# Performance work log

Hardware: AMD Instinct MI355X
Metric: run time of the kernel (lower is better)

Reference implementation:

```python
import jax, jax.numpy as jnp
import numpy as np

B, S, D, H, KD, HID = 8, 1024, 512, 8, 64, 32


def setup_inputs() -> dict:
    key = jax.random.key(0)
    ks = jax.random.split(key, 13)
    s = 0.05
    return {
        "src": jax.random.normal(ks[0], (B, S, D), jnp.float32),
        "Wq": jax.random.normal(ks[1], (H, KD, D), jnp.float32) * s,
        "Wk": jax.random.normal(ks[2], (H, KD, D), jnp.float32) * s,
        "Wv": jax.random.normal(ks[3], (H, KD, D), jnp.float32) * s,
        "c_raw": jnp.ones((H,), jnp.float32),              # nn.Parameter(1.0) per head
        "L": jnp.full((H,), 2.0, jnp.float32),             # nn.Parameter(2.0) per head
        "w1": jax.random.normal(ks[4], (H, HID), jnp.float32) * s,   # Linear(1,HID) weight
        "b1": jax.random.normal(ks[5], (H, HID), jnp.float32) * s,
        "W2": jax.random.normal(ks[6], (H, HID, HID), jnp.float32) * s,  # [out,in]
        "b2": jax.random.normal(ks[7], (H, HID), jnp.float32) * s,
        "w3": jax.random.normal(ks[8], (H, HID), jnp.float32) * s,   # Linear(HID,1) weight
        "b3": jax.random.normal(ks[9], (H,), jnp.float32) * s,
        "Wo": jax.random.normal(ks[10], (D, D), jnp.float32) * s,
    }


def _gelu(x):
    return jax.nn.gelu(x, approximate=False)  # torch nn.GELU default (erf)


def reference(src, Wq, Wk, Wv, c_raw, L, w1, b1, W2, b2, w3, b3, Wo):
    Bc, Sc, Dc = src.shape
    Hh, Kd = Wq.shape[0], Wq.shape[1]
    # ---- FIRE bias: raw[i,j] = log1p(c*(i-j)) / log1p(c*max(L, i+1)) for j<i else 0
    ii = jnp.arange(Sc, dtype=jnp.float32)[:, None]   # [S,1]
    jj = jnp.arange(Sc, dtype=jnp.float32)[None, :]   # [1,S]
    d = ii - jj                                       # [S,S]
    c = jax.nn.softplus(c_raw)[:, None, None]         # [H,1,1]
    num = jnp.log1p(c * jnp.where(d > 0, d, 1.0)[None])          # safe for d<=0
    den = jnp.log1p(c * jnp.maximum(L[:, None, None], ii[None] + 1.0))
    raw = jnp.where(d[None] > 0, num / den, 0.0)      # [H,S,S]
    # ---- f_theta MLP applied elementwise (Linear(1,h)->GELU->Linear(h,h)->GELU->Linear(h,1))
    h1 = _gelu(raw[..., None] * w1[:, None, None, :] + b1[:, None, None, :])   # [H,S,S,HID]
    h2 = _gelu(jnp.einsum('hijk,hlk->hijl', h1, W2) + b2[:, None, None, :])    # [H,S,S,HID]
    bias = jnp.einsum('hijk,hk->hij', h2, w3) + b3[:, None, None]              # [H,S,S]
    # ---- causal mask (strict upper triangle -> -inf)
    causal = jnp.arange(Sc)[None, :] > jnp.arange(Sc)[:, None]
    bias = jnp.where(causal[None], -jnp.inf, bias)
    # ---- attention per head
    q = jnp.einsum('bsd,hkd->bhsk', src, Wq)
    k = jnp.einsum('bsd,hkd->bhsk', src, Wk)
    v = jnp.einsum('bsd,hkd->bhsk', src, Wv)
    logits = jnp.einsum('bhik,bhjk->bhij', q, k) / jnp.sqrt(jnp.float32(Kd)) + bias[None]
    attn = jax.nn.softmax(logits, axis=-1)
    o = jnp.einsum('bhij,bhjk->bhik', attn, v)        # [B,H,S,KD]
    o = jnp.transpose(o, (0, 2, 1, 3)).reshape(Bc, Sc, Hh * Kd)  # concat heads
    return o @ Wo.T
```

## Files before the change

### kernel.cpp

```cpp
#include <hip/hip_runtime.h>
#include <math.h>

#define S_LEN 1024
#define NHEAD 8
#define BATCH 8
#define KDIM  64
#define HID   32
#define NT    2048
#define LOG2E 1.4426950408889634f
#define TRI(q) ((q) * ((q) + 1) / 2)
#define PERM(m) (((m) & 0x20) | (((m) & 0x0C) << 1) | (((m) & 0x10) >> 2) | ((m) & 3))
#define SWZ(row) (((((row) >> 3) & 1) << 2) | ((row) & 3))

typedef __attribute__((ext_vector_type(8))) short bf16x8;
typedef __attribute__((ext_vector_type(4))) float f32x4;
typedef unsigned short ushort_t;

__device__ inline ushort_t f2bf(float f) {
  union { float f; unsigned u; } v; v.f = f;
  unsigned u = v.u;
  return (ushort_t)((u + 0x7FFFu + ((u >> 16) & 1u)) >> 16);
}
__device__ inline float bf2f(ushort_t u) {
  union { unsigned x; float f; } v; v.x = ((unsigned)u) << 16; return v.f;
}

__device__ inline void gl_lds16(const ushort_t* g, ushort_t* l) {
  __builtin_amdgcn_global_load_lds(
      (const __attribute__((address_space(1))) unsigned int*)g,
      (__attribute__((address_space(3))) unsigned int*)l, 16, 0, 0);
}

__global__ __launch_bounds__(256) void prep(
    const float* __restrict__ s, const float* __restrict__ wq,
    const float* __restrict__ wk, const float* __restrict__ wv,
    const float* __restrict__ wo,
    ushort_t* __restrict__ sb, ushort_t* __restrict__ wqb,
    ushort_t* __restrict__ wkb, ushort_t* __restrict__ wvb,
    ushort_t* __restrict__ wob,
    const float* __restrict__ c_raw, const float* __restrict__ Lp,
    const float* __restrict__ w1, const float* __restrict__ b1,
    const float* __restrict__ W2, const float* __restrict__ b2,
    const float* __restrict__ w3, const float* __restrict__ b3,
    float* __restrict__ num_g, float* __restrict__ rden_g,
    float* __restrict__ gtab_g) {
  __shared__ float h1s[8][33];
  const int bx = blockIdx.x;
  const int tid = threadIdx.x;
  if (bx < 5120) {
    const float* src; ushort_t* dst; int base; float scale = 1.0f;
    if (bx < 4096)      { src = s;  dst = sb;  base = bx; }
    else if (bx < 4352) { src = wq; dst = wqb; base = bx - 4096; scale = 0.125f * LOG2E; }
    else if (bx < 4608) { src = wk; dst = wkb; base = bx - 4352; }
    else if (bx < 4864) { src = wv; dst = wvb; base = bx - 4608; }
    else                { src = wo; dst = wob; base = bx - 4864; }
    const int i = (base * 256 + tid) * 4;
    float4 v = *(const float4*)&src[i];
    ushort4 o;
    o.x = f2bf(v.x * scale); o.y = f2bf(v.y * scale);
    o.z = f2bf(v.z * scale); o.w = f2bf(v.w * scale);
    *(ushort4*)&dst[i] = o;
  } else {
    const int idx = bx - 5120;
    const int h = idx / 257;
    const int xb = idx % 257;
    const float cr = c_raw[h];
    const float c = (cr > 20.f) ? cr : log1pf(expf(cr));
    const int gid = xb * 256 + tid;
    if (gid < S_LEN) {
      num_g[h * S_LEN + gid] = log1pf(c * (float)gid);
      rden_g[h * S_LEN + gid] = 1.0f / log1pf(c * fmaxf(Lp[h], (float)(gid + 1)));
    }
    const int pl = tid >> 5;
    const int j = tid & 31;
    const int pt = xb * 8 + pl;
    const float x = (float)pt * (1.0f / NT);
    float v = x * w1[h * HID + j] + b1[h * HID + j];
    h1s[pl][j] = 0.5f * v * (1.0f + erff(v * 0.70710678118f));
    __syncthreads();
    float sm = b2[h * HID + j];
    const float* w2r = W2 + ((size_t)(h * HID + j)) * HID;
    #pragma unroll
    for (int k = 0; k < HID; ++k) sm += w2r[k] * h1s[pl][k];
    float g = 0.5f * sm * (1.0f + erff(sm * 0.70710678118f));
    float y = w3[h * HID + j] * g;
    #pragma unroll
    for (int off = 1; off < 32; off <<= 1) y += __shfl_xor(y, off);
    if (j == 0 && pt <= NT) gtab_g[h * (NT + 1) + pt] = (y + b3[h]) * LOG2E;
  }
}

__device__ __forceinline__ void gemm_tile(
    ushort_t* sAB, const ushort_t* __restrict__ A, const ushort_t* __restrict__ Wp,
    void* __restrict__ outp, int mode, int m0, int n0, int tid) {
  const int lane = tid & 63, w = tid >> 6, quad = lane >> 4, l16 = lane & 15;
  f32x4 acc[4];
  #pragma unroll
  for (int nb = 0; nb < 4; ++nb) acc[nb] = (f32x4)0.0f;

  const int r8 = lane >> 3;
  const int gc = (lane & 7) ^ r8;
  const int sw = l16 & 7;

  auto stage = [&](int kt, int buf) {
    ushort_t* sA = sAB + buf * 8192;
    ushort_t* sB = sA + 4096;
    #pragma unroll
    for (int j = 0; j < 2; ++j) {
      const int row = w * 16 + j * 8 + r8;
      gl_lds16(&A[(size_t)(m0 + row) * 512 + kt + gc * 8], &sA[(w * 16 + j * 8) * 64]);
      gl_lds16(&Wp[(size_t)(n0 + row) * 512 + kt + gc * 8], &sB[(w * 16 + j * 8) * 64]);
    }
  };

  stage(0, 0);
  __syncthreads();
  for (int kt8 = 0; kt8 < 8; ++kt8) {
    const int cur = kt8 & 1;
    if (kt8 < 7) stage((kt8 + 1) * 64, cur ^ 1);
    const ushort_t* sA = sAB + cur * 8192;
    const ushort_t* sB = sA + 4096;
    #pragma unroll
    for (int ks = 0; ks < 2; ++ks) {
      const int off = ((ks * 4 + quad) ^ sw) * 8;
      bf16x8 af = *(const bf16x8*)&sA[(w * 16 + l16) * 64 + off];
      #pragma unroll
      for (int nb = 0; nb < 4; ++nb) {
        bf16x8 bfr = *(const bf16x8*)&sB[(nb * 16 + l16) * 64 + off];
        acc[nb] = __builtin_amdgcn_mfma_f32_16x16x32_bf16(af, bfr, acc[nb], 0, 0, 0);
      }
    }
    __syncthreads();
  }

  if (mode == 2) {
    #pragma unroll
    for (int nb = 0; nb < 4; ++nb)
      #pragma unroll
      for (int r = 0; r < 4; ++r) {
        int nl = nb * 16 + l16;
        int ml = w * 16 + quad * 4 + r;
        sAB[nl * 64 + (((ml >> 3) ^ (nl & 7)) * 8) + (ml & 7)] = f2bf(acc[nb][r]);
      }
    __syncthreads();
    const int nl = tid >> 2, seg = tid & 3;
    const int ng = n0 + nl, hh = ng >> 6, kd = ng & 63;
    const int bb = m0 >> 10, sbase = m0 & 1023;
    ushort_t* vout = (ushort_t*)outp + (((size_t)(bb * NHEAD + hh)) * KDIM + kd) * S_LEN;
    #pragma unroll
    for (int c2 = 0; c2 < 2; ++c2) {
      int mc = seg * 2 + c2;
      bf16x8 vr = *(bf16x8*)&sAB[nl * 64 + ((mc ^ (nl & 7)) * 8)];
      *(bf16x8*)&vout[sbase + mc * 8] = vr;
    }
    return;
  }
  #pragma unroll
  for (int nb = 0; nb < 4; ++nb) {
    #pragma unroll
    for (int r = 0; r < 4; ++r) {
      int m = m0 + w * 16 + quad * 4 + r;
      int n = n0 + nb * 16 + l16;
      float v = acc[nb][r];
      if (mode == 1) {
        int bb = m >> 10, ss = m & 1023, hh = n >> 6, kd = n & 63;
        ((ushort_t*)outp)[(((size_t)(bb * NHEAD + hh)) * S_LEN + ss) * KDIM + kd] = f2bf(v);
      } else {
        ((float*)outp)[(size_t)m * 512 + n] = v;
      }
    }
  }
}

__global__ __launch_bounds__(256) void gemm_bias(
    const ushort_t* __restrict__ A,
    const ushort_t* __restrict__ W0, const ushort_t* __restrict__ W1,
    const ushort_t* __restrict__ W2w,
    void* __restrict__ out0, void* __restrict__ out1, void* __restrict__ out2,
    int scatter, int nGemm,
    const float* __restrict__ num_g, const float* __restrict__ rden_g,
    const float* __restrict__ gtab_g, ushort_t* __restrict__ biaspre) {
  __shared__ __align__(16) ushort_t sAB[16384];
  const int tid = threadIdx.x;
  if ((int)blockIdx.x < nGemm) {
    int z, tile;
    if (scatter) { z = blockIdx.x % 3; tile = blockIdx.x / 3; }
    else         { z = 0;              tile = blockIdx.x; }
    const int m0 = (tile & 127) * 64;
    const int n0 = (tile >> 7) * 64;
    const ushort_t* Wp = (z == 0) ? W0 : (z == 1) ? W1 : W2w;
    void* outp = (z == 0) ? out0 : (z == 1) ? out1 : out2;
    const int mode = scatter ? ((z == 2) ? 2 : 1) : 0;
    gemm_tile(sAB, A, Wp, outp, mode, m0, n0, tid);
  } else {
    const int idx = blockIdx.x - nGemm;
    const int h = idx / 68;
    const int pair = idx % 68;
    float* gtab_s = (float*)sAB;
    float* num_s = gtab_s + 2052;
    float* rden_s = num_s + 1024;
    for (int i = tid; i <= NT; i += 256) gtab_s[i] = gtab_g[h * (NT + 1) + i];
    for (int i = tid; i < S_LEN; i += 256) num_s[i] = num_g[h * S_LEN + i];
    const int sub = tid >> 7, tid2 = tid & 127;
    const int tileIdx = pair * 2 + sub;
    int qt = 0;
    while (TRI(qt + 1) <= tileIdx) ++qt;
    const int t = tileIdx - TRI(qt);
    if (tid2 < 64) rden_s[sub * 64 + tid2] = rden_g[h * S_LEN + qt * 64 + tid2];
    __syncthreads();
    const int w = tid2 >> 6, lane = tid2 & 63, quad = lane >> 4, l16 = lane & 15;
    ushort_t vals[32];
    #pragma unroll
    for (int qg = 0; qg < 2; ++qg) {
      const int iloc = w * 32 + qg * 16 + l16;
      const int i = qt * 64 + iloc;
      const float rden = rden_s[sub * 64 + iloc];
      #pragma unroll
      for (int nb = 0; nb < 4; ++nb)
        #pragma unroll
        for (int r = 0; r < 4; ++r) {
          const int m = nb * 16 + quad * 4 + r;
          const int j = t * 64 + PERM(m);
          ushort_t out;
          if (j > i) {
            out = 0xFF80;
          } else {
            const int d = i - j;
            float x = num_s[d] * rden;
            float tf = x * (float)NT;
            int it = (int)tf; it = it < (NT - 1) ? it : (NT - 1);
            float fr = tf - (float)it;
            float ga = gtab_s[it];
            out = f2bf(ga + (gtab_s[it + 1] - ga) * fr);
          }
          vals[qg * 16 + nb * 4 + r] = out;
        }
    }
    ushort_t* dst = &biaspre[((size_t)(h * 136 + tileIdx) * 128 + tid2) * 32];
    uint4 u[2];
    #pragma unroll
    for (int half = 0; half < 2; ++half) {
      #pragma unroll
      for (int v = 0; v < 8; ++v) ((ushort_t*)&u[0])[v] = vals[half * 16 + v];
      #pragma unroll
      for (int v = 0; v < 8; ++v) ((ushort_t*)&u[1])[v] = vals[half * 16 + 8 + v];
      *(uint4*)(dst + half * 16) = u[0];
      *(uint4*)(dst + half * 16 + 8) = u[1];
    }
  }
}

__global__ __launch_bounds__(128) void fire_attn_mfma(
    const ushort_t* __restrict__ Qg, const ushort_t* __restrict__ Kg,
    const ushort_t* __restrict__ Vtg, const ushort_t* __restrict__ biaspre,
    ushort_t* __restrict__ Ob) {
  __shared__ __align__(16) ushort_t Ks[2 * 64 * 64];
  __shared__ __align__(16) ushort_t Vt[2 * 64 * 64];
  const int tid = threadIdx.x;
  const int lane = tid & 63, w = tid >> 6, quad = lane >> 4, l16 = lane & 15;
  const int g = blockIdx.x >> 6;
  const int qt = (g < 8) ? (15 - g) : (g - 8);
  const int bh = blockIdx.x & 63, h = bh & 7, b = bh >> 3;

  bf16x8 q[2][2];
  {
    const size_t qb = (size_t)bh * S_LEN + qt * 64 + w * 32;
    #pragma unroll
    for (int qg = 0; qg < 2; ++qg)
      #pragma unroll
      for (int ks = 0; ks < 2; ++ks)
        q[qg][ks] = *(const bf16x8*)&Qg[(qb + qg * 16 + l16) * KDIM + ks * 32 + quad * 8];
  }

  const size_t kb = (size_t)bh * S_LEN * KDIM;
  const ushort_t* bptr = &biaspre[((size_t)(h * 136 + TRI(qt)) * 128 + tid) * 32];
  const int srow8 = lane >> 3;
  const int sc = lane & 7;

  auto stageKV = [&](int t, int buf) {
    #pragma unroll
    for (int j = 0; j < 4; ++j) {
      const int row = (w * 4 + j) * 8 + srow8;
      const int cc = sc ^ SWZ(row);
      gl_lds16(&Kg[kb + (size_t)(t * 64 + row) * 64 + cc * 8],
               &Ks[buf * 4096 + (w * 4 + j) * 512]);
      gl_lds16(&Vtg[kb + (size_t)row * 1024 + t * 64 + cc * 8],
               &Vt[buf * 4096 + (w * 4 + j) * 512]);
    }
  };

  f32x4 o[2][4];
  float ll[2] = {0.f, 0.f};
  #pragma unroll
  for (int qg = 0; qg < 2; ++qg)
    #pragma unroll
    for (int nb = 0; nb < 4; ++nb) o[qg][nb] = (f32x4)0.0f;

  stageKV(0, 0);
  __syncthreads();
  for (int t = 0; t <= qt; ++t) {
    const int cur = t & 1;
    if (t < qt) stageKV(t + 1, cur ^ 1);
    const ushort_t* Kc = Ks + cur * 4096;
    const ushort_t* Vc = Vt + cur * 4096;

    uint4 bb0 = ((const uint4*)(bptr + (size_t)t * 4096))[0];
    uint4 bb1 = ((const uint4*)(bptr + (size_t)t * 4096))[1];
    uint4 bb2 = ((const uint4*)(bptr + (size_t)t * 4096))[2];
    uint4 bb3 = ((const uint4*)(bptr + (size_t)t * 4096))[3];

    f32x4 s[2][4];
    #pragma unroll
    for (int qg = 0; qg < 2; ++qg)
      #pragma unroll
      for (int nb = 0; nb < 4; ++nb) s[qg][nb] = (f32x4)0.0f;
    #pragma unroll
    for (int ks = 0; ks < 2; ++ks) {
      #pragma unroll
      for (int nb = 0; nb < 4; ++nb) {
        const int rk = PERM(nb * 16 + l16);
        bf16x8 ak = *(const bf16x8*)&Kc[rk * 64 + (((ks * 4 + quad) ^ SWZ(rk)) * 8)];
        #pragma unroll
        for (int qg = 0; qg < 2; ++qg)
          s[qg][nb] = __builtin_amdgcn_mfma_f32_16x16x32_bf16(ak, q[qg][ks], s[qg][nb], 0, 0, 0);
      }
    }

    unsigned pk[2][4][2];
    #pragma unroll
    for (int qg = 0; qg < 2; ++qg) {
      #pragma unroll
      for (int nb = 0; nb < 4; ++nb) {
        const int v = qg * 16 + nb * 4;
        const uint4& bq = (v < 8) ? bb0 : (v < 16) ? bb1 : (v < 24) ? bb2 : bb3;
        const ushort_t* bu = (const ushort_t*)&bq;
        float p0 = __builtin_amdgcn_exp2f(s[qg][nb][0] + bf2f(bu[(v + 0) & 7]));
        float p1 = __builtin_amdgcn_exp2f(s[qg][nb][1] + bf2f(bu[(v + 1) & 7]));
        float p2 = __builtin_amdgcn_exp2f(s[qg][nb][2] + bf2f(bu[(v + 2) & 7]));
        float p3 = __builtin_amdgcn_exp2f(s[qg][nb][3] + bf2f(bu[(v + 3) & 7]));
        ll[qg] += (p0 + p1) + (p2 + p3);
        asm("v_cvt_pk_bf16_f32 %0, %1, %2" : "=v"(pk[qg][nb][0]) : "v"(p0), "v"(p1));
        asm("v_cvt_pk_bf16_f32 %0, %1, %2" : "=v"(pk[qg][nb][1]) : "v"(p2), "v"(p3));
      }
    }

    #pragma unroll
    for (int ks = 0; ks < 2; ++ks) {
      bf16x8 pf[2];
      #pragma unroll
      for (int qg = 0; qg < 2; ++qg) {
        union { bf16x8 v; unsigned u[4]; } pkx;
        pkx.u[0] = pk[qg][2 * ks][0];
        pkx.u[1] = pk[qg][2 * ks][1];
        pkx.u[2] = pk[qg][2 * ks + 1][0];
        pkx.u[3] = pk[qg][2 * ks + 1][1];
        pf[qg] = pkx.v;
      }
      #pragma unroll
      for (int nb = 0; nb < 4; ++nb) {
        const int rv = nb * 16 + l16;
        bf16x8 av = *(const bf16x8*)&Vc[rv * 64 + (((ks * 4 + quad) ^ SWZ(rv)) * 8)];
        #pragma unroll
        for (int qg = 0; qg < 2; ++qg)
          o[qg][nb] = __builtin_amdgcn_mfma_f32_16x16x32_bf16(av, pf[qg], o[qg][nb], 0, 0, 0);
      }
    }
    __syncthreads();
  }

  #pragma unroll
  for (int qg = 0; qg < 2; ++qg) {
    float rs = ll[qg];
    rs += __shfl_xor(rs, 16);
    rs += __shfl_xor(rs, 32);
    const float rl = 1.0f / rs;
    const size_t ob = ((size_t)(b * S_LEN + qt * 64 + w * 32 + qg * 16 + l16)) * 512 + h * KDIM;
    #pragma unroll
    for (int nb = 0; nb < 4; ++nb) {
      ushort4 ov;
      ov.x = f2bf(o[qg][nb][0] * rl);
      ov.y = f2bf(o[qg][nb][1] * rl);
      ov.z = f2bf(o[qg][nb][2] * rl);
      ov.w = f2bf(o[qg][nb][3] * rl);
      *(ushort4*)&Ob[ob + nb * 16 + quad * 4] = ov;
    }
  }
}

extern "C" void kernel_launch(void* const* d_in, const int* in_sizes, int n_in,
                              void* d_out, int out_size, void* d_ws, size_t ws_size,
                              hipStream_t stream) {
  const float* src   = (const float*)d_in[0];
  const float* Wq    = (const float*)d_in[1];
  const float* Wk    = (const float*)d_in[2];
  const float* Wv    = (const float*)d_in[3];
  const float* c_raw = (const float*)d_in[4];
  const float* Lp    = (const float*)d_in[5];
  const float* w1    = (const float*)d_in[6];
  const float* b1    = (const float*)d_in[7];
  const float* W2    = (const float*)d_in[8];
  const float* b2    = (const float*)d_in[9];
  const float* w3    = (const float*)d_in[10];
  const float* b3    = (const float*)d_in[11];
  const float* Wo    = (const float*)d_in[12];
  float* outp = (float*)d_out;

  const size_t SRC_E = 4194304;
  const size_t W_E   = 262144;
  const size_t QKV_E = 4194304;
  ushort_t* srcb = (ushort_t*)d_ws;
  ushort_t* Wqb  = srcb + SRC_E;
  ushort_t* Wkb  = Wqb + W_E;
  ushort_t* Wvb  = Wkb + W_E;
  ushort_t* Wob  = Wvb + W_E;
  ushort_t* Qb   = Wob + W_E;
  ushort_t* Kb   = Qb + QKV_E;
  ushort_t* Vtb  = Kb + QKV_E;
  ushort_t* Obb  = Vtb + QKV_E;
  ushort_t* biaspre = Obb + QKV_E;
  float* numb  = (float*)(biaspre + (size_t)NHEAD * 136 * 128 * 32);
  float* rdenb = numb + NHEAD * S_LEN;
  float* gtabb = rdenb + NHEAD * S_LEN;

  hipLaunchKernelGGL(prep, dim3(7176), dim3(256), 0, stream,
                     src, Wq, Wk, Wv, Wo, srcb, Wqb, Wkb, Wvb, Wob,
                     c_raw, Lp, w1, b1, W2, b2, w3, b3, numb, rdenb, gtabb);
  hipLaunchKernelGGL(gemm_bias, dim3(3616), dim3(256), 0, stream,
                     srcb, Wqb, Wkb, Wvb, (void*)Qb, (void*)Kb, (void*)Vtb,
                     1, 3072, numb, rdenb, gtabb, biaspre);
  hipLaunchKernelGGL(fire_attn_mfma, dim3(1024), dim3(128), 0, stream,
                     Qb, Kb, Vtb, biaspre, Obb);
  hipLaunchKernelGGL(gemm_bias, dim3(1024), dim3(256), 0, stream,
                     Obb, Wob, Wob, Wob, (void*)outp, (void*)outp, (void*)outp,
                     0, 1024, numb, rdenb, gtabb, biaspre);
}
```

Before: 167.3 us.

## Fuse fp32-to-bf16 conversion of src into the QKV projection GEMM

Removes the separate src fp32->bf16 conversion pass from the prep kernel and its bf16 workspace copy. The QKV GEMM now loads fp32 src tiles into registers, converts them with packed bf16 conversion, and writes them into swizzled LDS, overlapping the next tile's loads with the current MFMA work. This avoids writing and re-reading the 8 MB bf16 src buffer. In exchange, the QKV GEMM reads twice as many bytes of A per tile (fp32, read by three z-blocks) and uses register staging instead of direct global-to-LDS loads.

New measurement: 183.5 us. +9.7%, slower.

```diff
diff --git a/kernel.cpp b/kernel.cpp
--- a/kernel.cpp
+++ b/kernel.cpp
@@ -24,6 +24,11 @@
 __device__ inline float bf2f(ushort_t u) {
   union { unsigned x; float f; } v; v.x = ((unsigned)u) << 16; return v.f;
 }
+__device__ inline unsigned cvtpk_bf16(float lo, float hi) {
+  unsigned r;
+  asm("v_cvt_pk_bf16_f32 %0, %1, %2" : "=v"(r) : "v"(lo), "v"(hi));
+  return r;
+}
 
 __device__ inline void gl_lds16(const ushort_t* g, ushort_t* l) {
   __builtin_amdgcn_global_load_lds(
@@ -32,10 +37,10 @@
 }
 
 __global__ __launch_bounds__(256) void prep(
-    const float* __restrict__ s, const float* __restrict__ wq,
+    const float* __restrict__ wq,
     const float* __restrict__ wk, const float* __restrict__ wv,
     const float* __restrict__ wo,
-    ushort_t* __restrict__ sb, ushort_t* __restrict__ wqb,
+    ushort_t* __restrict__ wqb,
     ushort_t* __restrict__ wkb, ushort_t* __restrict__ wvb,
     ushort_t* __restrict__ wob,
     const float* __restrict__ c_raw, const float* __restrict__ Lp,
@@ -47,13 +52,12 @@
   __shared__ float h1s[8][33];
   const int bx = blockIdx.x;
   const int tid = threadIdx.x;
-  if (bx < 5120) {
+  if (bx < 1024) {
     const float* src; ushort_t* dst; int base; float scale = 1.0f;
-    if (bx < 4096)      { src = s;  dst = sb;  base = bx; }
-    else if (bx < 4352) { src = wq; dst = wqb; base = bx - 4096; scale = 0.125f * LOG2E; }
-    else if (bx < 4608) { src = wk; dst = wkb; base = bx - 4352; }
-    else if (bx < 4864) { src = wv; dst = wvb; base = bx - 4608; }
-    else                { src = wo; dst = wob; base = bx - 4864; }
+    if (bx < 256)      { src = wq; dst = wqb; base = bx;       scale = 0.125f * LOG2E; }
+    else if (bx < 512) { src = wk; dst = wkb; base = bx - 256; }
+    else if (bx < 768) { src = wv; dst = wvb; base = bx - 512; }
+    else               { src = wo; dst = wob; base = bx - 768; }
     const int i = (base * 256 + tid) * 4;
     float4 v = *(const float4*)&src[i];
     ushort4 o;
@@ -61,7 +65,7 @@
     o.z = f2bf(v.z * scale); o.w = f2bf(v.w * scale);
     *(ushort4*)&dst[i] = o;
   } else {
-    const int idx = bx - 5120;
+    const int idx = bx - 1024;
     const int h = idx / 257;
     const int xb = idx % 257;
     const float cr = c_raw[h];
@@ -90,8 +94,9 @@
   }
 }
 
+template <bool AF32>
 __device__ __forceinline__ void gemm_tile(
-    ushort_t* sAB, const ushort_t* __restrict__ A, const ushort_t* __restrict__ Wp,
+    ushort_t* sAB, const void* __restrict__ Ap, const ushort_t* __restrict__ Wp,
     void* __restrict__ outp, int mode, int m0, int n0, int tid) {
   const int lane = tid & 63, w = tid >> 6, quad = lane >> 4, l16 = lane & 15;
   f32x4 acc[4];
@@ -99,25 +104,70 @@
   for (int nb = 0; nb < 4; ++nb) acc[nb] = (f32x4)0.0f;
 
   const int r8 = lane >> 3;
-  const int gc = (lane & 7) ^ r8;
+  const int c8 = lane & 7;
+  const int gc = c8 ^ r8;
   const int sw = l16 & 7;
 
-  auto stage = [&](int kt, int buf) {
+  float4 rA0[2], rA1[2];
+
+  auto stageA_issue = [&](int kt) {
+    if (AF32) {
+      const float* Af = (const float*)Ap;
+      {
+        const float* p = &Af[(size_t)(m0 + w * 16 + r8) * 512 + kt + c8 * 8];
+        rA0[0] = *(const float4*)p; rA0[1] = *(const float4*)(p + 4);
+      }
+      {
+        const float* p = &Af[(size_t)(m0 + w * 16 + 8 + r8) * 512 + kt + c8 * 8];
+        rA1[0] = *(const float4*)p; rA1[1] = *(const float4*)(p + 4);
+      }
+    }
+  };
+  auto stageA_write = [&](int buf) {
     ushort_t* sA = sAB + buf * 8192;
-    ushort_t* sB = sA + 4096;
     #pragma unroll
     for (int j = 0; j < 2; ++j) {
       const int row = w * 16 + j * 8 + r8;
-      gl_lds16(&A[(size_t)(m0 + row) * 512 + kt + gc * 8], &sA[(w * 16 + j * 8) * 64]);
+      float4 a = j ? rA1[0] : rA0[0];
+      float4 b = j ? rA1[1] : rA0[1];
+      union { bf16x8 v; unsigned u[4]; } pk8;
+      pk8.u[0] = cvtpk_bf16(a.x, a.y);
+      pk8.u[1] = cvtpk_bf16(a.z, a.w);
+      pk8.u[2] = cvtpk_bf16(b.x, b.y);
+      pk8.u[3] = cvtpk_bf16(b.z, b.w);
+      *(bf16x8*)&sA[row * 64 + (c8 ^ r8) * 8] = pk8.v;
+    }
+  };
+  auto stageA_lds = [&](int kt, int buf) {
+    ushort_t* sA = sAB + buf * 8192;
+    const ushort_t* Ab = (const ushort_t*)Ap;
+    #pragma unroll
+    for (int j = 0; j < 2; ++j) {
+      const int row = w * 16 + j * 8 + r8;
+      gl_lds16(&Ab[(size_t)(m0 + row) * 512 + kt + gc * 8], &sA[(w * 16 + j * 8) * 64]);
+    }
+  };
+  auto stageW = [&](int kt, int buf) {
+    ushort_t* sB = sAB + buf * 8192 + 4096;
+    #pragma unroll
+    for (int j = 0; j < 2; ++j) {
+      const int row = w * 16 + j * 8 + r8;
       gl_lds16(&Wp[(size_t)(n0 + row) * 512 + kt + gc * 8], &sB[(w * 16 + j * 8) * 64]);
     }
   };
 
-  stage(0, 0);
+  stageA_issue(0);
+  stageW(0, 0);
+  if (AF32) stageA_write(0); else stageA_lds(0, 0);
   __syncthreads();
+
   for (int kt8 = 0; kt8 < 8; ++kt8) {
     const int cur = kt8 & 1;
-    if (kt8 < 7) stage((kt8 + 1) * 64, cur ^ 1);
+    if (kt8 < 7) {
+      stageA_issue((kt8 + 1) * 64);
+      stageW((kt8 + 1) * 64, cur ^ 1);
+      if (!AF32) stageA_lds((kt8 + 1) * 64, cur ^ 1);
+    }
     const ushort_t* sA = sAB + cur * 8192;
     const ushort_t* sB = sA + 4096;
     #pragma unroll
@@ -130,6 +180,7 @@
         acc[nb] = __builtin_amdgcn_mfma_f32_16x16x32_bf16(af, bfr, acc[nb], 0, 0, 0);
       }
     }
+    if (AF32 && kt8 < 7) stageA_write(cur ^ 1);
     __syncthreads();
   }
 
@@ -173,7 +224,7 @@
 }
 
 __global__ __launch_bounds__(256) void gemm_bias(
-    const ushort_t* __restrict__ A,
+    const float* __restrict__ Af32, const ushort_t* __restrict__ Abf,
     const ushort_t* __restrict__ W0, const ushort_t* __restrict__ W1,
     const ushort_t* __restrict__ W2w,
     void* __restrict__ out0, void* __restrict__ out1, void* __restrict__ out2,
@@ -190,8 +241,11 @@
     const int n0 = (tile >> 7) * 64;
     const ushort_t* Wp = (z == 0) ? W0 : (z == 1) ? W1 : W2w;
     void* outp = (z == 0) ? out0 : (z == 1) ? out1 : out2;
-    const int mode = scatter ? ((z == 2) ? 2 : 1) : 0;
-    gemm_tile(sAB, A, Wp, outp, mode, m0, n0, tid);
+    if (scatter) {
+      gemm_tile<true>(sAB, (const void*)Af32, Wp, outp, (z == 2) ? 2 : 1, m0, n0, tid);
+    } else {
+      gemm_tile<false>(sAB, (const void*)Abf, Wp, outp, 0, m0, n0, tid);
+    }
   } else {
     const int idx = blockIdx.x - nGemm;
     const int h = idx / 68;
@@ -339,8 +393,8 @@
         float p2 = __builtin_amdgcn_exp2f(s[qg][nb][2] + bf2f(bu[(v + 2) & 7]));
         float p3 = __builtin_amdgcn_exp2f(s[qg][nb][3] + bf2f(bu[(v + 3) & 7]));
         ll[qg] += (p0 + p1) + (p2 + p3);
-        asm("v_cvt_pk_bf16_f32 %0, %1, %2" : "=v"(pk[qg][nb][0]) : "v"(p0), "v"(p1));
-        asm("v_cvt_pk_bf16_f32 %0, %1, %2" : "=v"(pk[qg][nb][1]) : "v"(p2), "v"(p3));
+        pk[qg][nb][0] = cvtpk_bf16(p0, p1);
+        pk[qg][nb][1] = cvtpk_bf16(p2, p3);
       }
     }
 
@@ -405,11 +459,9 @@
   const float* Wo    = (const float*)d_in[12];
   float* outp = (float*)d_out;
 
-  const size_t SRC_E = 4194304;
   const size_t W_E   = 262144;
   const size_t QKV_E = 4194304;
-  ushort_t* srcb = (ushort_t*)d_ws;
-  ushort_t* Wqb  = srcb + SRC_E;
+  ushort_t* Wqb  = (ushort_t*)d_ws;
   ushort_t* Wkb  = Wqb + W_E;
   ushort_t* Wvb  = Wkb + W_E;
   ushort_t* Wob  = Wvb + W_E;
@@ -422,15 +474,17 @@
   float* rdenb = numb + NHEAD * S_LEN;
   float* gtabb = rdenb + NHEAD * S_LEN;
 
-  hipLaunchKernelGGL(prep, dim3(7176), dim3(256), 0, stream,
-                     src, Wq, Wk, Wv, Wo, srcb, Wqb, Wkb, Wvb, Wob,
+  hipLaunchKernelGGL(prep, dim3(3080), dim3(256), 0, stream,
+                     Wq, Wk, Wv, Wo, Wqb, Wkb, Wvb, Wob,
                      c_raw, Lp, w1, b1, W2, b2, w3, b3, numb, rdenb, gtabb);
   hipLaunchKernelGGL(gemm_bias, dim3(3616), dim3(256), 0, stream,
-                     srcb, Wqb, Wkb, Wvb, (void*)Qb, (void*)Kb, (void*)Vtb,
+                     src, (const ushort_t*)nullptr, Wqb, Wkb, Wvb,
+                     (void*)Qb, (void*)Kb, (void*)Vtb,
                      1, 3072, numb, rdenb, gtabb, biaspre);
   hipLaunchKernelGGL(fire_attn_mfma, dim3(1024), dim3(128), 0, stream,
                      Qb, Kb, Vtb, biaspre, Obb);
   hipLaunchKernelGGL(gemm_bias, dim3(1024), dim3(256), 0, stream,
-                     Obb, Wob, Wob, Wob, (void*)outp, (void*)outp, (void*)outp,
+                     (const float*)nullptr, Obb, Wob, Wob, Wob,
+                     (void*)outp, (void*)outp, (void*)outp,
                      0, 1024, numb, rdenb, gtabb, biaspre);
 }
```
